# Optimization experiments

Measured on AMD Instinct MI355X. Metric: run time of the kernel, lower is better.

## Reference

```python
import jax, jax.numpy as jnp
import numpy as np

B = 64          # batch == number of parallel fc layers used
T = 512         # sequence length
IN_FEATS = 1024
OUT_FEATS = 1024


def setup_inputs() -> dict:
    key = jax.random.key(0)
    kx, kw, kb = jax.random.split(key, 3)
    x = jax.random.normal(kx, (B, T, IN_FEATS), dtype=jnp.float32)
    # Per-sample Linear weights, stacked: W[i] is the weight of list_fc[i]
    # (torch Linear weight layout: [out_feats, in_feats])
    bound = 1.0 / np.sqrt(IN_FEATS)
    W = jax.random.uniform(kw, (B, OUT_FEATS, IN_FEATS), dtype=jnp.float32,
                           minval=-bound, maxval=bound)
    b = jax.random.uniform(kb, (B, OUT_FEATS), dtype=jnp.float32,
                           minval=-bound, maxval=bound)
    return {"x": x, "W": W, "b": b}


def reference(x, W, b):
    # Equivalent to: cat([list_fc[i](x[i:i+1]) for i in range(B)], dim=0)
    # i.e. a grouped GEMM with group size 1: out[i] = x[i] @ W[i].T + b[i]
    out = jnp.einsum('bti,boi->bto', x, W)  # [B, T, OUT]
    return out + b[:, None, :]
```

## Files before the change

kernel.cpp:

```cpp
#include <hip/hip_runtime.h>
#include <hip/hip_bf16.h>

#define BATCH 64
#define MDIM 512
#define NDIM 1024
#define KDIM 1024

#define BM 256
#define BN 256
#define BK 64
#define NKT (KDIM / BK)

typedef __attribute__((ext_vector_type(4))) float f32x4;
typedef __attribute__((ext_vector_type(8))) short bf16x8;
typedef __attribute__((ext_vector_type(4))) unsigned int u32x4;

__device__ __forceinline__ unsigned int cvt2(float lo, float hi) {
    __hip_bfloat162 h = __float22bfloat162_rn(float2{lo, hi});
    return *(unsigned int*)&h;
}

#define MFMA16(a, b, c) __builtin_amdgcn_mfma_f32_16x16x32_bf16((a), (b), (c), 0, 0, 0)

#define TILE_SEAL do { \
    asm volatile("s_waitcnt lgkmcnt(0)" ::: "memory"); \
    __builtin_amdgcn_sched_barrier(0); \
    __builtin_amdgcn_s_barrier(); \
    __builtin_amdgcn_sched_barrier(0); } while (0)

__global__ __launch_bounds__(512, 2)
void grouped_fc_kernel(const float* __restrict__ X,
                       const float* __restrict__ W,
                       const float* __restrict__ Bias,
                       float* __restrict__ Out) {
    const int swz  = (blockIdx.x & 7) * 64 + (blockIdx.x >> 3);
    const int bidx = swz >> 3;
    const int tile = swz & 7;
    const int tm = tile & 1;
    const int tn = tile >> 1;

    const int tid  = threadIdx.x;
    const int lane = tid & 63;
    const int wid  = tid >> 6;
    const int wm   = wid & 1;
    const int wn   = wid >> 1;

    __shared__ unsigned short ldsA[2][BM][BK];
    __shared__ unsigned short ldsB[2][BN][BK];

    const float* srcA = X + ((size_t)bidx * MDIM + (size_t)tm * BM) * KDIM;
    const float* srcB = W + ((size_t)bidx * NDIM + (size_t)tn * BN) * KDIM;

    const int s_r  = tid >> 2;
    const int s_cf = (tid & 3) * 16;
    const int s_x  = s_r & 7;
    const int so0  = (((tid & 3) * 2)     ^ s_x) * 8;
    const int so1  = (((tid & 3) * 2 + 1) ^ s_x) * 8;

    f32x4 st0[4], st1[4];

    auto ISSUE = [&](const float* srcbase, int hv, int kt_, f32x4 (&s)[4]) {
        const float* p = srcbase + (size_t)(hv * 128 + s_r) * KDIM + kt_ * BK + s_cf;
#pragma unroll
        for (int v = 0; v < 4; ++v) s[v] = *(const f32x4*)(p + v * 4);
    };

    auto CVTW = [&](unsigned short* ldsbase, int hv, f32x4 (&s)[4]) {
        const int row = hv * 128 + s_r;
        u32x4 w0, w1;
        w0[0] = cvt2(s[0][0], s[0][1]); w0[1] = cvt2(s[0][2], s[0][3]);
        w0[2] = cvt2(s[1][0], s[1][1]); w0[3] = cvt2(s[1][2], s[1][3]);
        w1[0] = cvt2(s[2][0], s[2][1]); w1[1] = cvt2(s[2][2], s[2][3]);
        w1[2] = cvt2(s[3][0], s[3][1]); w1[3] = cvt2(s[3][2], s[3][3]);
        *(u32x4*)&ldsbase[(size_t)row * BK + so0] = w0;
        *(u32x4*)&ldsbase[(size_t)row * BK + so1] = w1;
    };

    const int frow = lane & 15;
    const int khi  = lane >> 4;
    const int xr   = frow & 7;
    const int oK0  = ((khi)     ^ xr) * 8;
    const int oK1  = ((4 + khi) ^ xr) * 8;

    f32x4 acc[8][4];
#pragma unroll
    for (int mi = 0; mi < 8; ++mi)
#pragma unroll
        for (int ni = 0; ni < 4; ++ni)
            acc[mi][ni] = (f32x4){0.f, 0.f, 0.f, 0.f};

    ISSUE(srcA, 0, 0, st0); ISSUE(srcA, 1, 0, st1);
    CVTW(&ldsA[0][0][0], 0, st0); CVTW(&ldsA[0][0][0], 1, st1);
    ISSUE(srcB, 0, 0, st0); ISSUE(srcB, 1, 0, st1);
    CVTW(&ldsB[0][0][0], 0, st0); CVTW(&ldsB[0][0][0], 1, st1);
    TILE_SEAL;

#pragma unroll 1
    for (int kt = 0; kt < NKT; ++kt) {
        const int rd = kt & 1;
        const bool m1 = (kt + 1 < NKT);
        unsigned short* nA = &ldsA[rd ^ 1][0][0];
        unsigned short* nB = &ldsB[rd ^ 1][0][0];
        bf16x8 af[8], bfr[4];

        if (m1) { ISSUE(srcA, 0, kt + 1, st0); ISSUE(srcA, 1, kt + 1, st1); }

#pragma unroll
        for (int mi = 0; mi < 8; ++mi)
            af[mi] = *(const bf16x8*)&ldsA[rd][wm * 128 + mi * 16 + frow][oK0];
#pragma unroll
        for (int ni = 0; ni < 4; ++ni)
            bfr[ni] = *(const bf16x8*)&ldsB[rd][wn * 64 + ni * 16 + frow][oK0];

        __builtin_amdgcn_s_setprio(1);
#pragma unroll
        for (int mi = 0; mi < 8; ++mi)
#pragma unroll
            for (int ni = 0; ni < 4; ++ni)
                acc[mi][ni] = MFMA16(af[mi], bfr[ni], acc[mi][ni]);
        __builtin_amdgcn_s_setprio(0);

        if (m1) {
            CVTW(nA, 0, st0); CVTW(nA, 1, st1);
            ISSUE(srcB, 0, kt + 1, st0); ISSUE(srcB, 1, kt + 1, st1);
        }

#pragma unroll
        for (int mi = 0; mi < 8; ++mi)
            af[mi] = *(const bf16x8*)&ldsA[rd][wm * 128 + mi * 16 + frow][oK1];
#pragma unroll
        for (int ni = 0; ni < 4; ++ni)
            bfr[ni] = *(const bf16x8*)&ldsB[rd][wn * 64 + ni * 16 + frow][oK1];

        __builtin_amdgcn_s_setprio(1);
#pragma unroll
        for (int mi = 0; mi < 8; ++mi)
#pragma unroll
            for (int ni = 0; ni < 4; ++ni)
                acc[mi][ni] = MFMA16(af[mi], bfr[ni], acc[mi][ni]);
        __builtin_amdgcn_s_setprio(0);

        if (m1) { CVTW(nB, 0, st0); CVTW(nB, 1, st1); }

        TILE_SEAL;
    }

#pragma unroll
    for (int ni = 0; ni < 4; ++ni) {
        const int gc = tn * BN + wn * 64 + ni * 16 + frow;
        const float bv = Bias[bidx * NDIM + gc];
#pragma unroll
        for (int mi = 0; mi < 8; ++mi) {
            const int gr0 = tm * BM + wm * 128 + mi * 16 + (lane >> 4) * 4;
            float* po = Out + ((size_t)bidx * MDIM + gr0) * NDIM + gc;
#pragma unroll
            for (int r = 0; r < 4; ++r)
                po[(size_t)r * NDIM] = acc[mi][ni][r] + bv;
        }
    }
}

extern "C" void kernel_launch(void* const* d_in, const int* in_sizes, int n_in,
                              void* d_out, int out_size, void* d_ws, size_t ws_size,
                              hipStream_t stream) {
    const float* X  = (const float*)d_in[0];
    const float* W  = (const float*)d_in[1];
    const float* Bs = (const float*)d_in[2];
    float* Out = (float*)d_out;

    grouped_fc_kernel<<<dim3(512), dim3(512), 0, stream>>>(X, W, Bs, Out);
}
```

Baseline: 150.0 us.

## Shrink tiles to 256x128x32 with 4x2 warp grid for higher occupancy

```diff
diff --git a/kernel.cpp b/kernel.cpp
--- a/kernel.cpp
+++ b/kernel.cpp
@@ -7,8 +7,8 @@
 #define KDIM 1024
 
 #define BM 256
-#define BN 256
-#define BK 64
+#define BN 128
+#define BK 32
 #define NKT (KDIM / BK)
 
 typedef __attribute__((ext_vector_type(4))) float f32x4;
@@ -28,22 +28,22 @@
     __builtin_amdgcn_s_barrier(); \
     __builtin_amdgcn_sched_barrier(0); } while (0)
 
-__global__ __launch_bounds__(512, 2)
+__global__ __launch_bounds__(512, 4)
 void grouped_fc_kernel(const float* __restrict__ X,
                        const float* __restrict__ W,
                        const float* __restrict__ Bias,
                        float* __restrict__ Out) {
-    const int swz  = (blockIdx.x & 7) * 64 + (blockIdx.x >> 3);
-    const int bidx = swz >> 3;
-    const int tile = swz & 7;
+    const int swz  = (blockIdx.x & 7) * 128 + (blockIdx.x >> 3);
+    const int bidx = swz >> 4;
+    const int tile = swz & 15;
     const int tm = tile & 1;
     const int tn = tile >> 1;
 
     const int tid  = threadIdx.x;
     const int lane = tid & 63;
     const int wid  = tid >> 6;
-    const int wm   = wid & 1;
-    const int wn   = wid >> 1;
+    const int wm   = wid & 3;
+    const int wn   = wid >> 2;
 
     __shared__ unsigned short ldsA[2][BM][BK];
     __shared__ unsigned short ldsB[2][BN][BK];
@@ -51,96 +51,77 @@
     const float* srcA = X + ((size_t)bidx * MDIM + (size_t)tm * BM) * KDIM;
     const float* srcB = W + ((size_t)bidx * NDIM + (size_t)tn * BN) * KDIM;
 
-    const int s_r  = tid >> 2;
-    const int s_cf = (tid & 3) * 16;
-    const int s_x  = s_r & 7;
-    const int so0  = (((tid & 3) * 2)     ^ s_x) * 8;
-    const int so1  = (((tid & 3) * 2 + 1) ^ s_x) * 8;
+    const int uA0 = tid, uA1 = tid + 512, uB = tid;
+    const int rA0 = uA0 >> 2, sA0 = uA0 & 3;
+    const int rA1 = uA1 >> 2, sA1 = uA1 & 3;
+    const int rB  = uB  >> 2, sB  = uB  & 3;
+    const int wA0 = (sA0 ^ ((rA0 >> 1) & 3)) * 8;
+    const int wA1 = (sA1 ^ ((rA1 >> 1) & 3)) * 8;
+    const int wB  = (sB  ^ ((rB  >> 1) & 3)) * 8;
 
-    f32x4 st0[4], st1[4];
+    f32x4 fa0[2], fa1[2], fb[2];
 
-    auto ISSUE = [&](const float* srcbase, int hv, int kt_, f32x4 (&s)[4]) {
-        const float* p = srcbase + (size_t)(hv * 128 + s_r) * KDIM + kt_ * BK + s_cf;
-#pragma unroll
-        for (int v = 0; v < 4; ++v) s[v] = *(const f32x4*)(p + v * 4);
+    auto ISSUE = [&](int kt) {
+        const float* p0 = srcA + (size_t)rA0 * KDIM + kt * BK + sA0 * 8;
+        const float* p1 = srcA + (size_t)rA1 * KDIM + kt * BK + sA1 * 8;
+        const float* pb = srcB + (size_t)rB  * KDIM + kt * BK + sB  * 8;
+        fa0[0] = *(const f32x4*)(p0); fa0[1] = *(const f32x4*)(p0 + 4);
+        fa1[0] = *(const f32x4*)(p1); fa1[1] = *(const f32x4*)(p1 + 4);
+        fb[0]  = *(const f32x4*)(pb); fb[1]  = *(const f32x4*)(pb + 4);
     };
 
-    auto CVTW = [&](unsigned short* ldsbase, int hv, f32x4 (&s)[4]) {
-        const int row = hv * 128 + s_r;
-        u32x4 w0, w1;
-        w0[0] = cvt2(s[0][0], s[0][1]); w0[1] = cvt2(s[0][2], s[0][3]);
-        w0[2] = cvt2(s[1][0], s[1][1]); w0[3] = cvt2(s[1][2], s[1][3]);
-        w1[0] = cvt2(s[2][0], s[2][1]); w1[1] = cvt2(s[2][2], s[2][3]);
-        w1[2] = cvt2(s[3][0], s[3][1]); w1[3] = cvt2(s[3][2], s[3][3]);
-        *(u32x4*)&ldsbase[(size_t)row * BK + so0] = w0;
-        *(u32x4*)&ldsbase[(size_t)row * BK + so1] = w1;
+    auto CVTW = [&](int buf) {
+        u32x4 w0, w1, w2;
+        w0[0] = cvt2(fa0[0][0], fa0[0][1]); w0[1] = cvt2(fa0[0][2], fa0[0][3]);
+        w0[2] = cvt2(fa0[1][0], fa0[1][1]); w0[3] = cvt2(fa0[1][2], fa0[1][3]);
+        w1[0] = cvt2(fa1[0][0], fa1[0][1]); w1[1] = cvt2(fa1[0][2], fa1[0][3]);
+        w1[2] = cvt2(fa1[1][0], fa1[1][1]); w1[3] = cvt2(fa1[1][2], fa1[1][3]);
+        w2[0] = cvt2(fb[0][0],  fb[0][1]);  w2[1] = cvt2(fb[0][2],  fb[0][3]);
+        w2[2] = cvt2(fb[1][0],  fb[1][1]);  w2[3] = cvt2(fb[1][2],  fb[1][3]);
+        *(u32x4*)&ldsA[buf][rA0][wA0] = w0;
+        *(u32x4*)&ldsA[buf][rA1][wA1] = w1;
+        *(u32x4*)&ldsB[buf][rB][wB]   = w2;
     };
 
     const int frow = lane & 15;
     const int khi  = lane >> 4;
-    const int xr   = frow & 7;
-    const int oK0  = ((khi)     ^ xr) * 8;
-    const int oK1  = ((4 + khi) ^ xr) * 8;
+    const int rsl  = (khi ^ ((frow >> 1) & 3)) * 8;
 
-    f32x4 acc[8][4];
+    f32x4 acc[4][4];
 #pragma unroll
-    for (int mi = 0; mi < 8; ++mi)
+    for (int mi = 0; mi < 4; ++mi)
 #pragma unroll
         for (int ni = 0; ni < 4; ++ni)
             acc[mi][ni] = (f32x4){0.f, 0.f, 0.f, 0.f};
 
-    ISSUE(srcA, 0, 0, st0); ISSUE(srcA, 1, 0, st1);
-    CVTW(&ldsA[0][0][0], 0, st0); CVTW(&ldsA[0][0][0], 1, st1);
-    ISSUE(srcB, 0, 0, st0); ISSUE(srcB, 1, 0, st1);
-    CVTW(&ldsB[0][0][0], 0, st0); CVTW(&ldsB[0][0][0], 1, st1);
+    ISSUE(0);
+    CVTW(0);
     TILE_SEAL;
 
 #pragma unroll 1
     for (int kt = 0; kt < NKT; ++kt) {
         const int rd = kt & 1;
         const bool m1 = (kt + 1 < NKT);
-        unsigned short* nA = &ldsA[rd ^ 1][0][0];
-        unsigned short* nB = &ldsB[rd ^ 1][0][0];
-        bf16x8 af[8], bfr[4];
 
-        if (m1) { ISSUE(srcA, 0, kt + 1, st0); ISSUE(srcA, 1, kt + 1, st1); }
+        if (m1) ISSUE(kt + 1);
 
+        bf16x8 af[4], bfr[4];
 #pragma unroll
-        for (int mi = 0; mi < 8; ++mi)
-            af[mi] = *(const bf16x8*)&ldsA[rd][wm * 128 + mi * 16 + frow][oK0];
+        for (int mi = 0; mi < 4; ++mi)
+            af[mi] = *(const bf16x8*)&ldsA[rd][wm * 64 + mi * 16 + frow][rsl];
 #pragma unroll
         for (int ni = 0; ni < 4; ++ni)
-            bfr[ni] = *(const bf16x8*)&ldsB[rd][wn * 64 + ni * 16 + frow][oK0];
+            bfr[ni] = *(const bf16x8*)&ldsB[rd][wn * 64 + ni * 16 + frow][rsl];
 
         __builtin_amdgcn_s_setprio(1);
 #pragma unroll
-        for (int mi = 0; mi < 8; ++mi)
+        for (int mi = 0; mi < 4; ++mi)
 #pragma unroll
             for (int ni = 0; ni < 4; ++ni)
                 acc[mi][ni] = MFMA16(af[mi], bfr[ni], acc[mi][ni]);
         __builtin_amdgcn_s_setprio(0);
 
-        if (m1) {
-            CVTW(nA, 0, st0); CVTW(nA, 1, st1);
-            ISSUE(srcB, 0, kt + 1, st0); ISSUE(srcB, 1, kt + 1, st1);
-        }
-
-#pragma unroll
-        for (int mi = 0; mi < 8; ++mi)
-            af[mi] = *(const bf16x8*)&ldsA[rd][wm * 128 + mi * 16 + frow][oK1];
-#pragma unroll
-        for (int ni = 0; ni < 4; ++ni)
-            bfr[ni] = *(const bf16x8*)&ldsB[rd][wn * 64 + ni * 16 + frow][oK1];
-
-        __builtin_amdgcn_s_setprio(1);
-#pragma unroll
-        for (int mi = 0; mi < 8; ++mi)
-#pragma unroll
-            for (int ni = 0; ni < 4; ++ni)
-                acc[mi][ni] = MFMA16(af[mi], bfr[ni], acc[mi][ni]);
-        __builtin_amdgcn_s_setprio(0);
-
-        if (m1) { CVTW(nB, 0, st0); CVTW(nB, 1, st1); }
+        if (m1) CVTW(rd ^ 1);
 
         TILE_SEAL;
     }
@@ -150,8 +131,8 @@
         const int gc = tn * BN + wn * 64 + ni * 16 + frow;
         const float bv = Bias[bidx * NDIM + gc];
 #pragma unroll
-        for (int mi = 0; mi < 8; ++mi) {
-            const int gr0 = tm * BM + wm * 128 + mi * 16 + (lane >> 4) * 4;
+        for (int mi = 0; mi < 4; ++mi) {
+            const int gr0 = tm * BM + wm * 64 + mi * 16 + khi * 4;
             float* po = Out + ((size_t)bidx * MDIM + gr0) * NDIM + gc;
 #pragma unroll
             for (int r = 0; r < 4; ++r)
@@ -168,5 +149,5 @@
     const float* Bs = (const float*)d_in[2];
     float* Out = (float*)d_out;
 
-    grouped_fc_kernel<<<dim3(512), dim3(512), 0, stream>>>(X, W, Bs, Out);
+    grouped_fc_kernel<<<dim3(1024), dim3(512), 0, stream>>>(X, W, Bs, Out);
 }
```

Result: slower. 209.0 us (+39.4%).

## Restructure K-loop into four interleaved MFMA phases with deeper global prefetch

Applied to the files above, without the earlier changes.

```diff
diff --git a/kernel.cpp b/kernel.cpp
--- a/kernel.cpp
+++ b/kernel.cpp
@@ -21,12 +21,9 @@
 }
 
 #define MFMA16(a, b, c) __builtin_amdgcn_mfma_f32_16x16x32_bf16((a), (b), (c), 0, 0, 0)
-
-#define TILE_SEAL do { \
-    asm volatile("s_waitcnt lgkmcnt(0)" ::: "memory"); \
-    __builtin_amdgcn_sched_barrier(0); \
-    __builtin_amdgcn_s_barrier(); \
-    __builtin_amdgcn_sched_barrier(0); } while (0)
+#define SB0 __builtin_amdgcn_sched_barrier(0)
+#define WAITLG(n) do { asm volatile("s_waitcnt lgkmcnt(" #n ")" ::: "memory"); SB0; } while (0)
+#define BAR do { SB0; __builtin_amdgcn_s_barrier(); SB0; } while (0)
 
 __global__ __launch_bounds__(512, 2)
 void grouped_fc_kernel(const float* __restrict__ X,
@@ -82,6 +79,13 @@
     const int oK0  = ((khi)     ^ xr) * 8;
     const int oK1  = ((4 + khi) ^ xr) * 8;
 
+    auto rdA = [&](int buf, int mi, int o) {
+        return *(const bf16x8*)&ldsA[buf][wm * 128 + mi * 16 + frow][o];
+    };
+    auto rdB = [&](int buf, int ni, int o) {
+        return *(const bf16x8*)&ldsB[buf][wn * 64 + ni * 16 + frow][o];
+    };
+
     f32x4 acc[8][4];
 #pragma unroll
     for (int mi = 0; mi < 8; ++mi)
@@ -93,56 +97,103 @@
     CVTW(&ldsA[0][0][0], 0, st0); CVTW(&ldsA[0][0][0], 1, st1);
     ISSUE(srcB, 0, 0, st0); ISSUE(srcB, 1, 0, st1);
     CVTW(&ldsB[0][0][0], 0, st0); CVTW(&ldsB[0][0][0], 1, st1);
-    TILE_SEAL;
+    ISSUE(srcA, 0, 1, st0); ISSUE(srcA, 1, 1, st1);
+    WAITLG(0);
+    BAR;
+
+    bf16x8 af[8], bfr[4];
 
 #pragma unroll 1
-    for (int kt = 0; kt < NKT; ++kt) {
+    for (int kt = 0; kt < NKT - 1; ++kt) {
         const int rd = kt & 1;
-        const bool m1 = (kt + 1 < NKT);
+        const bool m2 = (kt + 2 < NKT);
         unsigned short* nA = &ldsA[rd ^ 1][0][0];
         unsigned short* nB = &ldsB[rd ^ 1][0][0];
-        bf16x8 af[8], bfr[4];
-
-        if (m1) { ISSUE(srcA, 0, kt + 1, st0); ISSUE(srcA, 1, kt + 1, st1); }
-
-#pragma unroll
-        for (int mi = 0; mi < 8; ++mi)
-            af[mi] = *(const bf16x8*)&ldsA[rd][wm * 128 + mi * 16 + frow][oK0];
-#pragma unroll
-        for (int ni = 0; ni < 4; ++ni)
-            bfr[ni] = *(const bf16x8*)&ldsB[rd][wn * 64 + ni * 16 + frow][oK0];
-
-        __builtin_amdgcn_s_setprio(1);
+
+#pragma unroll
+        for (int mi = 0; mi < 8; ++mi) af[mi] = rdA(rd, mi, oK0);
+        bfr[0] = rdB(rd, 0, oK0); bfr[1] = rdB(rd, 1, oK0);
+        WAITLG(0);
+        __builtin_amdgcn_s_setprio(1);
+#pragma unroll
+        for (int mi = 0; mi < 8; ++mi) {
+            acc[mi][0] = MFMA16(af[mi], bfr[0], acc[mi][0]);
+            acc[mi][1] = MFMA16(af[mi], bfr[1], acc[mi][1]);
+        }
+        __builtin_amdgcn_s_setprio(0);
+        SB0;
+        bfr[2] = rdB(rd, 2, oK0); bfr[3] = rdB(rd, 3, oK0);
+        CVTW(nA, 0, st0);
+        ISSUE(srcB, 0, kt + 1, st0);
+        BAR;
+
+        WAITLG(2);
+        __builtin_amdgcn_s_setprio(1);
+#pragma unroll
+        for (int mi = 0; mi < 8; ++mi) {
+            acc[mi][2] = MFMA16(af[mi], bfr[2], acc[mi][2]);
+            acc[mi][3] = MFMA16(af[mi], bfr[3], acc[mi][3]);
+        }
+        __builtin_amdgcn_s_setprio(0);
+        SB0;
+#pragma unroll
+        for (int mi = 0; mi < 8; ++mi) af[mi] = rdA(rd, mi, oK1);
+        bfr[0] = rdB(rd, 0, oK1); bfr[1] = rdB(rd, 1, oK1);
+        CVTW(nA, 1, st1);
+        ISSUE(srcB, 1, kt + 1, st1);
+        BAR;
+
+        WAITLG(2);
+        __builtin_amdgcn_s_setprio(1);
+#pragma unroll
+        for (int mi = 0; mi < 8; ++mi) {
+            acc[mi][0] = MFMA16(af[mi], bfr[0], acc[mi][0]);
+            acc[mi][1] = MFMA16(af[mi], bfr[1], acc[mi][1]);
+        }
+        __builtin_amdgcn_s_setprio(0);
+        SB0;
+        bfr[2] = rdB(rd, 2, oK1); bfr[3] = rdB(rd, 3, oK1);
+        CVTW(nB, 0, st0);
+        if (m2) ISSUE(srcA, 0, kt + 2, st0);
+        BAR;
+
+        WAITLG(2);
+        __builtin_amdgcn_s_setprio(1);
+#pragma unroll
+        for (int mi = 0; mi < 8; ++mi) {
+            acc[mi][2] = MFMA16(af[mi], bfr[2], acc[mi][2]);
+            acc[mi][3] = MFMA16(af[mi], bfr[3], acc[mi][3]);
+        }
+        __builtin_amdgcn_s_setprio(0);
+        SB0;
+        CVTW(nB, 1, st1);
+        if (m2) ISSUE(srcA, 1, kt + 2, st1);
+        WAITLG(0);
+        BAR;
+    }
+
+    {
+        const int rd = (NKT - 1) & 1;
+#pragma unroll
+        for (int mi = 0; mi < 8; ++mi) af[mi] = rdA(rd, mi, oK0);
+#pragma unroll
+        for (int ni = 0; ni < 4; ++ni) bfr[ni] = rdB(rd, ni, oK0);
+        WAITLG(0);
 #pragma unroll
         for (int mi = 0; mi < 8; ++mi)
 #pragma unroll
             for (int ni = 0; ni < 4; ++ni)
                 acc[mi][ni] = MFMA16(af[mi], bfr[ni], acc[mi][ni]);
-        __builtin_amdgcn_s_setprio(0);
-
-        if (m1) {
-            CVTW(nA, 0, st0); CVTW(nA, 1, st1);
-            ISSUE(srcB, 0, kt + 1, st0); ISSUE(srcB, 1, kt + 1, st1);
-        }
-
-#pragma unroll
-        for (int mi = 0; mi < 8; ++mi)
-            af[mi] = *(const bf16x8*)&ldsA[rd][wm * 128 + mi * 16 + frow][oK1];
-#pragma unroll
-        for (int ni = 0; ni < 4; ++ni)
-            bfr[ni] = *(const bf16x8*)&ldsB[rd][wn * 64 + ni * 16 + frow][oK1];
-
-        __builtin_amdgcn_s_setprio(1);
+#pragma unroll
+        for (int mi = 0; mi < 8; ++mi) af[mi] = rdA(rd, mi, oK1);
+#pragma unroll
+        for (int ni = 0; ni < 4; ++ni) bfr[ni] = rdB(rd, ni, oK1);
+        WAITLG(0);
 #pragma unroll
         for (int mi = 0; mi < 8; ++mi)
 #pragma unroll
             for (int ni = 0; ni < 4; ++ni)
                 acc[mi][ni] = MFMA16(af[mi], bfr[ni], acc[mi][ni]);
-        __builtin_amdgcn_s_setprio(0);
-
-        if (m1) { CVTW(nB, 0, st0); CVTW(nB, 1, st1); }
-
-        TILE_SEAL;
     }
 
 #pragma unroll
@@ -151,7 +202,7 @@
         const float bv = Bias[bidx * NDIM + gc];
 #pragma unroll
         for (int mi = 0; mi < 8; ++mi) {
-            const int gr0 = tm * BM + wm * 128 + mi * 16 + (lane >> 4) * 4;
+            const int gr0 = tm * BM + wm * 128 + mi * 16 + khi * 4;
             float* po = Out + ((size_t)bidx * MDIM + gr0) * NDIM + gc;
 #pragma unroll
             for (int r = 0; r < 4; ++r)
```

Measured after the change: 138.5 us. 7.7% less time.

## Warp-specialize into producer and MFMA consumer waves with smaller N tile

Applied to the files above, without the earlier changes.

```diff
diff --git a/kernel.cpp b/kernel.cpp
--- a/kernel.cpp
+++ b/kernel.cpp
@@ -7,7 +7,7 @@
 #define KDIM 1024
 
 #define BM 256
-#define BN 256
+#define BN 128
 #define BK 64
 #define NKT (KDIM / BK)
 
@@ -21,29 +21,24 @@
 }
 
 #define MFMA16(a, b, c) __builtin_amdgcn_mfma_f32_16x16x32_bf16((a), (b), (c), 0, 0, 0)
-
-#define TILE_SEAL do { \
-    asm volatile("s_waitcnt lgkmcnt(0)" ::: "memory"); \
-    __builtin_amdgcn_sched_barrier(0); \
-    __builtin_amdgcn_s_barrier(); \
-    __builtin_amdgcn_sched_barrier(0); } while (0)
+#define SB0 __builtin_amdgcn_sched_barrier(0)
+#define WAITLG(n) do { asm volatile("s_waitcnt lgkmcnt(" #n ")" ::: "memory"); SB0; } while (0)
+#define BAR do { SB0; __builtin_amdgcn_s_barrier(); SB0; } while (0)
 
 __global__ __launch_bounds__(512, 2)
 void grouped_fc_kernel(const float* __restrict__ X,
                        const float* __restrict__ W,
                        const float* __restrict__ Bias,
                        float* __restrict__ Out) {
-    const int swz  = (blockIdx.x & 7) * 64 + (blockIdx.x >> 3);
-    const int bidx = swz >> 3;
-    const int tile = swz & 7;
+    const int swz  = (blockIdx.x & 7) * 128 + (blockIdx.x >> 3);
+    const int bidx = swz >> 4;
+    const int tile = swz & 15;
     const int tm = tile & 1;
     const int tn = tile >> 1;
 
     const int tid  = threadIdx.x;
     const int lane = tid & 63;
     const int wid  = tid >> 6;
-    const int wm   = wid & 1;
-    const int wn   = wid >> 1;
 
     __shared__ unsigned short ldsA[2][BM][BK];
     __shared__ unsigned short ldsB[2][BN][BK];
@@ -51,111 +46,126 @@
     const float* srcA = X + ((size_t)bidx * MDIM + (size_t)tm * BM) * KDIM;
     const float* srcB = W + ((size_t)bidx * NDIM + (size_t)tn * BN) * KDIM;
 
-    const int s_r  = tid >> 2;
-    const int s_cf = (tid & 3) * 16;
-    const int s_x  = s_r & 7;
-    const int so0  = (((tid & 3) * 2)     ^ s_x) * 8;
-    const int so1  = (((tid & 3) * 2 + 1) ^ s_x) * 8;
+    if (wid < 4) {
+        const int wm = wid & 1;
+        const int wn = wid >> 1;
+        const int frow = lane & 15;
+        const int khi  = lane >> 4;
+        const int xr   = frow & 7;
+        const int oK0  = ((khi)     ^ xr) * 8;
+        const int oK1  = ((4 + khi) ^ xr) * 8;
 
-    f32x4 st0[4], st1[4];
-
-    auto ISSUE = [&](const float* srcbase, int hv, int kt_, f32x4 (&s)[4]) {
-        const float* p = srcbase + (size_t)(hv * 128 + s_r) * KDIM + kt_ * BK + s_cf;
-#pragma unroll
-        for (int v = 0; v < 4; ++v) s[v] = *(const f32x4*)(p + v * 4);
-    };
-
-    auto CVTW = [&](unsigned short* ldsbase, int hv, f32x4 (&s)[4]) {
-        const int row = hv * 128 + s_r;
-        u32x4 w0, w1;
-        w0[0] = cvt2(s[0][0], s[0][1]); w0[1] = cvt2(s[0][2], s[0][3]);
-        w0[2] = cvt2(s[1][0], s[1][1]); w0[3] = cvt2(s[1][2], s[1][3]);
-        w1[0] = cvt2(s[2][0], s[2][1]); w1[1] = cvt2(s[2][2], s[2][3]);
-        w1[2] = cvt2(s[3][0], s[3][1]); w1[3] = cvt2(s[3][2], s[3][3]);
-        *(u32x4*)&ldsbase[(size_t)row * BK + so0] = w0;
-        *(u32x4*)&ldsbase[(size_t)row * BK + so1] = w1;
-    };
-
-    const int frow = lane & 15;
-    const int khi  = lane >> 4;
-    const int xr   = frow & 7;
-    const int oK0  = ((khi)     ^ xr) * 8;
-    const int oK1  = ((4 + khi) ^ xr) * 8;
-
-    f32x4 acc[8][4];
-#pragma unroll
-    for (int mi = 0; mi < 8; ++mi)
-#pragma unroll
-        for (int ni = 0; ni < 4; ++ni)
-            acc[mi][ni] = (f32x4){0.f, 0.f, 0.f, 0.f};
-
-    ISSUE(srcA, 0, 0, st0); ISSUE(srcA, 1, 0, st1);
-    CVTW(&ldsA[0][0][0], 0, st0); CVTW(&ldsA[0][0][0], 1, st1);
-    ISSUE(srcB, 0, 0, st0); ISSUE(srcB, 1, 0, st1);
-    CVTW(&ldsB[0][0][0], 0, st0); CVTW(&ldsB[0][0][0], 1, st1);
-    TILE_SEAL;
-
-#pragma unroll 1
-    for (int kt = 0; kt < NKT; ++kt) {
-        const int rd = kt & 1;
-        const bool m1 = (kt + 1 < NKT);
-        unsigned short* nA = &ldsA[rd ^ 1][0][0];
-        unsigned short* nB = &ldsB[rd ^ 1][0][0];
-        bf16x8 af[8], bfr[4];
-
-        if (m1) { ISSUE(srcA, 0, kt + 1, st0); ISSUE(srcA, 1, kt + 1, st1); }
-
-#pragma unroll
-        for (int mi = 0; mi < 8; ++mi)
-            af[mi] = *(const bf16x8*)&ldsA[rd][wm * 128 + mi * 16 + frow][oK0];
-#pragma unroll
-        for (int ni = 0; ni < 4; ++ni)
-            bfr[ni] = *(const bf16x8*)&ldsB[rd][wn * 64 + ni * 16 + frow][oK0];
-
-        __builtin_amdgcn_s_setprio(1);
+        f32x4 acc[8][4];
 #pragma unroll
         for (int mi = 0; mi < 8; ++mi)
 #pragma unroll
             for (int ni = 0; ni < 4; ++ni)
-                acc[mi][ni] = MFMA16(af[mi], bfr[ni], acc[mi][ni]);
-        __builtin_amdgcn_s_setprio(0);
+                acc[mi][ni] = (f32x4){0.f, 0.f, 0.f, 0.f};
 
-        if (m1) {
-            CVTW(nA, 0, st0); CVTW(nA, 1, st1);
-            ISSUE(srcB, 0, kt + 1, st0); ISSUE(srcB, 1, kt + 1, st1);
+        BAR;
+
+        bf16x8 af[8], bfr[4];
+#pragma unroll 1
+        for (int kt = 0; kt < NKT; ++kt) {
+            const int rd = kt & 1;
+#pragma unroll
+            for (int mi = 0; mi < 8; ++mi)
+                af[mi] = *(const bf16x8*)&ldsA[rd][wm * 128 + mi * 16 + frow][oK0];
+#pragma unroll
+            for (int ni = 0; ni < 4; ++ni)
+                bfr[ni] = *(const bf16x8*)&ldsB[rd][wn * 64 + ni * 16 + frow][oK0];
+            WAITLG(0);
+            __builtin_amdgcn_s_setprio(1);
+#pragma unroll
+            for (int mi = 0; mi < 8; ++mi)
+#pragma unroll
+                for (int ni = 0; ni < 4; ++ni)
+                    acc[mi][ni] = MFMA16(af[mi], bfr[ni], acc[mi][ni]);
+            __builtin_amdgcn_s_setprio(0);
+            SB0;
+#pragma unroll
+            for (int mi = 0; mi < 8; ++mi)
+                af[mi] = *(const bf16x8*)&ldsA[rd][wm * 128 + mi * 16 + frow][oK1];
+#pragma unroll
+            for (int ni = 0; ni < 4; ++ni)
+                bfr[ni] = *(const bf16x8*)&ldsB[rd][wn * 64 + ni * 16 + frow][oK1];
+            WAITLG(0);
+            __builtin_amdgcn_s_setprio(1);
+#pragma unroll
+            for (int mi = 0; mi < 8; ++mi)
+#pragma unroll
+                for (int ni = 0; ni < 4; ++ni)
+                    acc[mi][ni] = MFMA16(af[mi], bfr[ni], acc[mi][ni]);
+            __builtin_amdgcn_s_setprio(0);
+            BAR;
         }
 
 #pragma unroll
-        for (int mi = 0; mi < 8; ++mi)
-            af[mi] = *(const bf16x8*)&ldsA[rd][wm * 128 + mi * 16 + frow][oK1];
+        for (int ni = 0; ni < 4; ++ni) {
+            const int gc = tn * BN + wn * 64 + ni * 16 + frow;
+            const float bv = Bias[bidx * NDIM + gc];
 #pragma unroll
-        for (int ni = 0; ni < 4; ++ni)
-            bfr[ni] = *(const bf16x8*)&ldsB[rd][wn * 64 + ni * 16 + frow][oK1];
+            for (int mi = 0; mi < 8; ++mi) {
+                const int gr0 = tm * BM + wm * 128 + mi * 16 + khi * 4;
+                float* po = Out + ((size_t)bidx * MDIM + gr0) * NDIM + gc;
+#pragma unroll
+                for (int r = 0; r < 4; ++r)
+                    po[(size_t)r * NDIM] = acc[mi][ni][r] + bv;
+            }
+        }
+    } else {
+        const int t = tid & 255;
+        const int rsub = t >> 3;
+        const int cg   = t & 7;
 
-        __builtin_amdgcn_s_setprio(1);
+        f32x4 pr[12][2];
+
+        auto STAGE = [&](int buf, int kt) {
 #pragma unroll
-        for (int mi = 0; mi < 8; ++mi)
+            for (int u = 0; u < 8; ++u) {
+                const int row = u * 32 + rsub;
+                const float* p = srcA + (size_t)row * KDIM + kt * BK + cg * 8;
+                pr[u][0] = *(const f32x4*)(p);
+                pr[u][1] = *(const f32x4*)(p + 4);
+            }
 #pragma unroll
-            for (int ni = 0; ni < 4; ++ni)
-                acc[mi][ni] = MFMA16(af[mi], bfr[ni], acc[mi][ni]);
-        __builtin_amdgcn_s_setprio(0);
+            for (int u = 8; u < 12; ++u) {
+                const int row = (u - 8) * 32 + rsub;
+                const float* p = srcB + (size_t)row * KDIM + kt * BK + cg * 8;
+                pr[u][0] = *(const f32x4*)(p);
+                pr[u][1] = *(const f32x4*)(p + 4);
+            }
+#pragma unroll
+            for (int u = 0; u < 8; ++u) {
+                const int row = u * 32 + rsub;
+                u32x4 w;
+                w[0] = cvt2(pr[u][0][0], pr[u][0][1]);
+                w[1] = cvt2(pr[u][0][2], pr[u][0][3]);
+                w[2] = cvt2(pr[u][1][0], pr[u][1][1]);
+                w[3] = cvt2(pr[u][1][2], pr[u][1][3]);
+                *(u32x4*)&ldsA[buf][row][(cg ^ (row & 7)) * 8] = w;
+            }
+#pragma unroll
+            for (int u = 8; u < 12; ++u) {
+                const int row = (u - 8) * 32 + rsub;
+                u32x4 w;
+                w[0] = cvt2(pr[u][0][0], pr[u][0][1]);
+                w[1] = cvt2(pr[u][0][2], pr[u][0][3]);
+                w[2] = cvt2(pr[u][1][0], pr[u][1][1]);
+                w[3] = cvt2(pr[u][1][2], pr[u][1][3]);
+                *(u32x4*)&ldsB[buf][row][(cg ^ (row & 7)) * 8] = w;
+            }
+        };
 
-        if (m1) { CVTW(nB, 0, st0); CVTW(nB, 1, st1); }
+        STAGE(0, 0);
+        WAITLG(0);
+        BAR;
 
-        TILE_SEAL;
-    }
-
-#pragma unroll
-    for (int ni = 0; ni < 4; ++ni) {
-        const int gc = tn * BN + wn * 64 + ni * 16 + frow;
-        const float bv = Bias[bidx * NDIM + gc];
-#pragma unroll
-        for (int mi = 0; mi < 8; ++mi) {
-            const int gr0 = tm * BM + wm * 128 + mi * 16 + (lane >> 4) * 4;
-            float* po = Out + ((size_t)bidx * MDIM + gr0) * NDIM + gc;
-#pragma unroll
-            for (int r = 0; r < 4; ++r)
-                po[(size_t)r * NDIM] = acc[mi][ni][r] + bv;
+#pragma unroll 1
+        for (int kt = 0; kt < NKT; ++kt) {
+            if (kt + 1 < NKT) STAGE((kt & 1) ^ 1, kt + 1);
+            WAITLG(0);
+            BAR;
         }
     }
 }
@@ -168,5 +178,5 @@
     const float* Bs = (const float*)d_in[2];
     float* Out = (float*)d_out;
 
-    grouped_fc_kernel<<<dim3(512), dim3(512), 0, stream>>>(X, W, Bs, Out);
+    grouped_fc_kernel<<<dim3(1024), dim3(512), 0, stream>>>(X, W, Bs, Out);
 }
```

Measured after the change: 193.6 us. +29.0%, slower.
